# Performance work log

Hardware: AMD Instinct MI355X
Metric: run time of the kernel (lower is better)

Reference implementation:

```python
import jax, jax.numpy as jnp
import numpy as np

KNN = 16
BN_EPS = 1e-5


def _swiglu(z, w1, w2, w3):
    # SwiGLU applied over the last dim: w2(silu(w1 z) * (w3 z))
    return (jax.nn.silu(z @ w1.T) * (z @ w3.T)) @ w2.T


def setup_inputs() -> dict:
    key = jax.random.key(0)
    ks = jax.random.split(key, 12)
    B, T, D = 1, 2048, 768
    H, N, KD = 4, 25600, 128
    HID_A, HID_S = 44, 1024
    inp = {
        "x": jax.random.normal(ks[0], (B, T, D), jnp.float32),
        "wq": jax.random.normal(ks[1], (H * KD, D), jnp.float32) * (1.0 / np.sqrt(D)),
        "bq": jax.random.normal(ks[2], (H * KD,), jnp.float32) * 0.02,
        "bn_gamma": jnp.ones((H * KD,), jnp.float32),
        "bn_beta": jnp.zeros((H * KD,), jnp.float32),
        "bn_mean": jnp.zeros((H * KD,), jnp.float32),
        "bn_var": jnp.ones((H * KD,), jnp.float32),
        "keys": jax.random.uniform(ks[3], (H, N, KD), jnp.float32, -1.0 / np.sqrt(KD), 1.0 / np.sqrt(KD)),
        "w_down_tab": jax.random.normal(ks[4], (N, 1), jnp.float32) * 0.02,
        "w_up_tab": jax.random.normal(ks[5], (N, 1), jnp.float32) * 0.02,
        "a_w1": jax.random.normal(ks[6], (HID_A, KNN), jnp.float32) * (1.0 / np.sqrt(KNN)),
        "a_w2": jax.random.normal(ks[7], (KNN, HID_A), jnp.float32) * (1.0 / np.sqrt(HID_A)),
        "a_w3": jax.random.normal(ks[8], (HID_A, KNN), jnp.float32) * (1.0 / np.sqrt(KNN)),
        "s_w1": jax.random.normal(ks[9], (HID_S, D), jnp.float32) * (1.0 / np.sqrt(D)),
        "s_w2": jax.random.normal(ks[10], (D, HID_S), jnp.float32) * (1.0 / np.sqrt(HID_S)),
        "s_w3": jax.random.normal(ks[11], (HID_S, D), jnp.float32) * (1.0 / np.sqrt(D)),
    }
    return inp


def reference(x, wq, bq, bn_gamma, bn_beta, bn_mean, bn_var, keys,
              w_down_tab, w_up_tab, a_w1, a_w2, a_w3, s_w1, s_w2, s_w3):
    B, T, D = x.shape
    H, N, KD = keys.shape
    identity = x
    # query projection + BatchNorm1d (inference: running stats)
    q = x.reshape(-1, D) @ wq.T + bq                      # (bs, H*KD)
    q = (q - bn_mean) * jax.lax.rsqrt(bn_var + BN_EPS) * bn_gamma + bn_beta
    q = q.reshape(-1, H, KD)                              # (bs, H, KD)
    # product-key scoring against full key table, per head
    scores = jnp.einsum('bhk,hnk->bhn', q, keys)          # (bs, H, N)
    top_s, top_i = jax.lax.top_k(scores, KNN)             # (bs, H, KNN)
    gates = jax.nn.softmax(top_s, axis=-1)
    idx = top_i.reshape(B, T, H, KNN)
    gates = gates.reshape(B, T, H, KNN)
    # expert_dim == 1: embedding gather yields a scalar per selected expert
    w_down = w_down_tab[idx, 0]                           # (B, T, H, KNN)
    w_up = w_up_tab[idx, 0]                               # (B, T, H, KNN)
    # einsum('btd,bthkd->bthk') with d-broadcast (expert_dim=1 vs D):
    # equals sum_d x[b,t,d] * w_down[b,t,h,k,0]
    xd = jnp.sum(x, axis=-1)[:, :, None, None] * w_down   # (B, T, H, KNN)
    h = _swiglu(xd, a_w1, a_w2, a_w3)                     # (B, T, H, KNN)
    h = h * gates
    # einsum('bthk,bthkd->btd') with d=1 -> (B, T, 1), broadcasts vs (B,T,D)
    comb = jnp.sum(h * w_up, axis=(2, 3))[:, :, None]     # (B, T, 1)
    out = comb + _swiglu(identity, s_w1, s_w2, s_w3)      # (B, T, D)
    return out
```

## Files before the change

kernel.cpp:

```cpp
#include <hip/hip_runtime.h>
#include <hip/hip_bf16.h>
#include <cmath>

#define NEG_INF (-3.402823466e38f)
#define SPLITS 32
#define SPN    800
#define GRP    32
#define NGRP   25

typedef __attribute__((ext_vector_type(8))) short s16x8;
typedef __attribute__((ext_vector_type(4))) float f32x4;

__device__ __forceinline__ unsigned short f2bf(float f) {
    union { float f; unsigned u; } v; v.f = f;
    unsigned u = v.u;
    u += 0x7fffu + ((u >> 16) & 1u);
    return (unsigned short)(u >> 16);
}

__global__ __launch_bounds__(256) void cvt_small_kernel(
        const float* __restrict__ s0, const float* __restrict__ s1,
        const float* __restrict__ s2, const float* __restrict__ s3,
        const float* __restrict__ s4,
        unsigned short* __restrict__ dst, float* __restrict__ sumx) {
    int i = blockIdx.x * 256 + threadIdx.x;
    const float* src; int base;
    if      (i < 393216)  { src = s0;   base = 0; }
    else if (i < 491520)  { src = s1;   base = 393216; }
    else if (i < 688128)  { src = s2;   base = 491520; }
    else if (i < 884736)  { src = s3;   base = 688128; }
    else                  { src = s4;   base = 884736; }
    float4 f = ((const float4*)src)[i - base];
    ushort4 o;
    o.x = f2bf(f.x); o.y = f2bf(f.y); o.z = f2bf(f.z); o.w = f2bf(f.w);
    ((ushort4*)dst)[i] = o;
    if (i < 393216) {
        float s = f.x + f.y + f.z + f.w;
        #pragma unroll
        for (int off = 32; off > 0; off >>= 1) s += __shfl_down(s, off);
        if ((threadIdx.x & 63) == 0) atomicAdd(&sumx[i / 192], s);
    }
}

__device__ __forceinline__ void qproj_body(
        int sb, int tid, const unsigned short* __restrict__ A,
        const unsigned short* __restrict__ W, unsigned short* __restrict__ outB,
        const float* __restrict__ bq, const float* __restrict__ gamma,
        const float* __restrict__ beta, const float* __restrict__ mean,
        const float* __restrict__ var, char* smem) {
    short (*As)[72] = (short(*)[72])smem;
    short (*Ws)[72] = (short(*)[72])(smem + 9216);
    const int m0 = (sb & 31) * 64, n0 = (sb >> 5) * 64;
    const int wv = tid >> 6, lane = tid & 63;
    const int wr = wv >> 1, wc = wv & 1;
    const int lr = lane & 15, lq = lane >> 4;
    f32x4 acc[2][2];
    #pragma unroll
    for (int i = 0; i < 2; ++i)
        #pragma unroll
        for (int j = 0; j < 2; ++j) acc[i][j] = (f32x4){0.f, 0.f, 0.f, 0.f};
    for (int kb = 0; kb < 768; kb += 64) {
        #pragma unroll
        for (int it = 0; it < 2; ++it) {
            int chunk = tid + it * 256;
            int row = chunk >> 3, c8 = (chunk & 7) * 8;
            *(s16x8*)&As[row][c8] = *(const s16x8*)(A + (size_t)(m0 + row) * 768 + kb + c8);
            *(s16x8*)&Ws[row][c8] = *(const s16x8*)(W + (size_t)(n0 + row) * 768 + kb + c8);
        }
        __syncthreads();
        #pragma unroll
        for (int ks = 0; ks < 2; ++ks) {
            const int k0 = ks * 32 + lq * 8;
            #pragma unroll
            for (int rt = 0; rt < 2; ++rt) {
                s16x8 a = *(const s16x8*)&As[wr * 32 + rt * 16 + lr][k0];
                #pragma unroll
                for (int ct = 0; ct < 2; ++ct) {
                    s16x8 b = *(const s16x8*)&Ws[wc * 32 + ct * 16 + lr][k0];
                    acc[rt][ct] = __builtin_amdgcn_mfma_f32_16x16x32_bf16(a, b, acc[rt][ct], 0, 0, 0);
                }
            }
        }
        __syncthreads();
    }
    #pragma unroll
    for (int rt = 0; rt < 2; ++rt)
        #pragma unroll
        for (int ct = 0; ct < 2; ++ct)
            #pragma unroll
            for (int r = 0; r < 4; ++r) {
                int m = m0 + wr * 32 + rt * 16 + lq * 4 + r;
                int n = n0 + wc * 32 + ct * 16 + lr;
                float q = acc[rt][ct][r] + bq[n];
                q = (q - mean[n]) * rsqrtf(var[n] + 1e-5f) * gamma[n] + beta[n];
                outB[(size_t)m * 512 + n] = f2bf(q);
            }
}

__global__ __launch_bounds__(256) void megaQ_kernel(
        const unsigned short* __restrict__ xb, const unsigned short* __restrict__ wqb,
        unsigned short* __restrict__ qb,
        const float* __restrict__ bq, const float* __restrict__ gamma,
        const float* __restrict__ beta, const float* __restrict__ mean,
        const float* __restrict__ var,
        const float* __restrict__ keys, unsigned short* __restrict__ keys_b) {
    __shared__ alignas(16) char smem[18432];
    if (blockIdx.x < 256) {
        qproj_body(blockIdx.x, threadIdx.x, xb, wqb, qb, bq, gamma, beta,
                   mean, var, smem);
    } else {
        int i = (blockIdx.x - 256) * 256 + threadIdx.x;
        float4 f = ((const float4*)keys)[i];
        ushort4 o;
        o.x = f2bf(f.x); o.y = f2bf(f.y); o.z = f2bf(f.z); o.w = f2bf(f.w);
        ((ushort4*)keys_b)[i] = o;
    }
}

template <int EPI>
__global__ __launch_bounds__(256) void gemm_nt(
        const unsigned short* __restrict__ A, const unsigned short* __restrict__ W,
        int M, int N, int K,
        float* __restrict__ outF, unsigned short* __restrict__ outB,
        const float* __restrict__ p0) {
    __shared__ alignas(16) short As[64][72];
    __shared__ alignas(16) short Ws[64][72];
    const int tid = threadIdx.x;
    const int m0 = blockIdx.x * 64, n0 = blockIdx.y * 64;
    const int wv = tid >> 6, lane = tid & 63;
    const int wr = wv >> 1, wc = wv & 1;
    const int lr = lane & 15, lq = lane >> 4;
    f32x4 acc[2][2];
    #pragma unroll
    for (int i = 0; i < 2; ++i)
        #pragma unroll
        for (int j = 0; j < 2; ++j) acc[i][j] = (f32x4){0.f, 0.f, 0.f, 0.f};

    for (int kb = 0; kb < K; kb += 64) {
        #pragma unroll
        for (int it = 0; it < 2; ++it) {
            int chunk = tid + it * 256;
            int row = chunk >> 3, c8 = (chunk & 7) * 8;
            *(s16x8*)&As[row][c8] = *(const s16x8*)(A + (size_t)(m0 + row) * K + kb + c8);
            *(s16x8*)&Ws[row][c8] = *(const s16x8*)(W + (size_t)(n0 + row) * K + kb + c8);
        }
        __syncthreads();
        #pragma unroll
        for (int ks = 0; ks < 2; ++ks) {
            const int k0 = ks * 32 + lq * 8;
            #pragma unroll
            for (int rt = 0; rt < 2; ++rt) {
                s16x8 a = *(const s16x8*)&As[wr * 32 + rt * 16 + lr][k0];
                #pragma unroll
                for (int ct = 0; ct < 2; ++ct) {
                    s16x8 b = *(const s16x8*)&Ws[wc * 32 + ct * 16 + lr][k0];
                    acc[rt][ct] = __builtin_amdgcn_mfma_f32_16x16x32_bf16(a, b, acc[rt][ct], 0, 0, 0);
                }
            }
        }
        __syncthreads();
    }
    #pragma unroll
    for (int rt = 0; rt < 2; ++rt)
        #pragma unroll
        for (int ct = 0; ct < 2; ++ct)
            #pragma unroll
            for (int r = 0; r < 4; ++r) {
                int m = m0 + wr * 32 + rt * 16 + lq * 4 + r;
                int n = n0 + wc * 32 + ct * 16 + lr;
                outF[(size_t)m * N + n] = acc[rt][ct][r] + p0[m];
            }
}

__device__ __forceinline__ void swiglu_body(
        int sb, int tid, const unsigned short* __restrict__ A,
        const unsigned short* __restrict__ W1, const unsigned short* __restrict__ W3,
        unsigned short* __restrict__ outB, char* smem) {
    short (*As)[72]  = (short(*)[72])smem;
    short (*W1s)[72] = (short(*)[72])(smem + 9216);
    short (*W3s)[72] = (short(*)[72])(smem + 18432);
    const int m0 = (sb & 31) * 64, n0 = (sb >> 5) * 64;
    const int wv = tid >> 6, lane = tid & 63;
    const int wr = wv >> 1, wc = wv & 1;
    const int lr = lane & 15, lq = lane >> 4;
    f32x4 acc1[2][2], acc3[2][2];
    #pragma unroll
    for (int i = 0; i < 2; ++i)
        #pragma unroll
        for (int j = 0; j < 2; ++j) {
            acc1[i][j] = (f32x4){0.f, 0.f, 0.f, 0.f};
            acc3[i][j] = (f32x4){0.f, 0.f, 0.f, 0.f};
        }
    for (int kb = 0; kb < 768; kb += 64) {
        #pragma unroll
        for (int it = 0; it < 2; ++it) {
            int chunk = tid + it * 256;
            int row = chunk >> 3, c8 = (chunk & 7) * 8;
            *(s16x8*)&As[row][c8]  = *(const s16x8*)(A  + (size_t)(m0 + row) * 768 + kb + c8);
            *(s16x8*)&W1s[row][c8] = *(const s16x8*)(W1 + (size_t)(n0 + row) * 768 + kb + c8);
            *(s16x8*)&W3s[row][c8] = *(const s16x8*)(W3 + (size_t)(n0 + row) * 768 + kb + c8);
        }
        __syncthreads();
        #pragma unroll
        for (int ks = 0; ks < 2; ++ks) {
            const int k0 = ks * 32 + lq * 8;
            #pragma unroll
            for (int rt = 0; rt < 2; ++rt) {
                s16x8 a = *(const s16x8*)&As[wr * 32 + rt * 16 + lr][k0];
                #pragma unroll
                for (int ct = 0; ct < 2; ++ct) {
                    s16x8 b1 = *(const s16x8*)&W1s[wc * 32 + ct * 16 + lr][k0];
                    s16x8 b3 = *(const s16x8*)&W3s[wc * 32 + ct * 16 + lr][k0];
                    acc1[rt][ct] = __builtin_amdgcn_mfma_f32_16x16x32_bf16(a, b1, acc1[rt][ct], 0, 0, 0);
                    acc3[rt][ct] = __builtin_amdgcn_mfma_f32_16x16x32_bf16(a, b3, acc3[rt][ct], 0, 0, 0);
                }
            }
        }
        __syncthreads();
    }
    #pragma unroll
    for (int rt = 0; rt < 2; ++rt)
        #pragma unroll
        for (int ct = 0; ct < 2; ++ct)
            #pragma unroll
            for (int r = 0; r < 4; ++r) {
                int m = m0 + wr * 32 + rt * 16 + lq * 4 + r;
                int n = n0 + wc * 32 + ct * 16 + lr;
                float u1 = acc1[rt][ct][r], u3 = acc3[rt][ct][r];
                float hv = u1 / (1.f + expf(-u1)) * u3;
                outB[(size_t)m * 1024 + n] = f2bf(hv);
            }
}

__device__ __forceinline__ void down_body(
        int sb, int tid, const unsigned short* __restrict__ A,
        const unsigned short* __restrict__ W, float* __restrict__ outF,
        char* smem) {
    short (*As)[72] = (short(*)[72])smem;
    short (*Ws)[72] = (short(*)[72])(smem + 9216);
    const int m0 = (sb & 31) * 64, n0 = (sb >> 5) * 64;
    const int wv = tid >> 6, lane = tid & 63;
    const int wr = wv >> 1, wc = wv & 1;
    const int lr = lane & 15, lq = lane >> 4;
    f32x4 acc[2][2];
    #pragma unroll
    for (int i = 0; i < 2; ++i)
        #pragma unroll
        for (int j = 0; j < 2; ++j) acc[i][j] = (f32x4){0.f, 0.f, 0.f, 0.f};
    for (int kb = 0; kb < 1024; kb += 64) {
        #pragma unroll
        for (int it = 0; it < 2; ++it) {
            int chunk = tid + it * 256;
            int row = chunk >> 3, c8 = (chunk & 7) * 8;
            *(s16x8*)&As[row][c8] = *(const s16x8*)(A + (size_t)(m0 + row) * 1024 + kb + c8);
            *(s16x8*)&Ws[row][c8] = *(const s16x8*)(W + (size_t)(n0 + row) * 1024 + kb + c8);
        }
        __syncthreads();
        #pragma unroll
        for (int ks = 0; ks < 2; ++ks) {
            const int k0 = ks * 32 + lq * 8;
            #pragma unroll
            for (int rt = 0; rt < 2; ++rt) {
                s16x8 a = *(const s16x8*)&As[wr * 32 + rt * 16 + lr][k0];
                #pragma unroll
                for (int ct = 0; ct < 2; ++ct) {
                    s16x8 b = *(const s16x8*)&Ws[wc * 32 + ct * 16 + lr][k0];
                    acc[rt][ct] = __builtin_amdgcn_mfma_f32_16x16x32_bf16(a, b, acc[rt][ct], 0, 0, 0);
                }
            }
        }
        __syncthreads();
    }
    #pragma unroll
    for (int rt = 0; rt < 2; ++rt)
        #pragma unroll
        for (int ct = 0; ct < 2; ++ct)
            #pragma unroll
            for (int r = 0; r < 4; ++r) {
                int m = m0 + wr * 32 + rt * 16 + lq * 4 + r;
                int n = n0 + wc * 32 + ct * 16 + lr;
                outF[(size_t)m * 768 + n] = acc[rt][ct][r];
            }
}

template <int PASS>
__device__ __forceinline__ void score_body(
        int b, int tid,
        const unsigned short* __restrict__ Q, const unsigned short* __restrict__ Kt,
        float* __restrict__ maxbuf, const float* __restrict__ theta,
        int* __restrict__ cnt, float2* __restrict__ buf, char* smem) {
    short (*Ks)[GRP][136] = (short(*)[GRP][136])smem;
    const int tile = b >> 7;
    const int hsp = b & 127;
    const int h = hsp >> 5, sp = hsp & 31;
    const int w = tid >> 6, lane = tid & 63;
    const int lr = lane & 15, lq = lane >> 4;
    const int t0 = tile * 256 + w * 64;
    const int nb0 = sp * SPN;

    s16x8 qf[4][4];
    #pragma unroll
    for (int tt = 0; tt < 4; ++tt) {
        const unsigned short* qp = Q + (size_t)(t0 + tt * 16 + lr) * 512 + h * 128 + lq * 8;
        #pragma unroll
        for (int ks = 0; ks < 4; ++ks) qf[tt][ks] = *(const s16x8*)(qp + ks * 32);
    }

    float runmax[4] = {NEG_INF, NEG_INF, NEG_INF, NEG_INF};
    float th[4];
    if (PASS == 2) {
        #pragma unroll
        for (int tt = 0; tt < 4; ++tt) th[tt] = theta[(t0 + tt * 16 + lr) * 4 + h];
    }

    const int srow = tid >> 4;
    const int scol = (tid & 15) * 8;
    const unsigned short* kgp =
        Kt + ((size_t)h * 25600 + nb0 + srow) * 128 + scol;

    {
        *(s16x8*)&Ks[0][srow][scol]      = *(const s16x8*)kgp;
        *(s16x8*)&Ks[0][srow + 16][scol] = *(const s16x8*)(kgp + 2048);
    }

    for (int g = 0; g < NGRP; ++g) {
        s16x8 ka0, ka1;
        if (g + 1 < NGRP) {
            const unsigned short* kp = kgp + (size_t)(g + 1) * 4096;
            ka0 = *(const s16x8*)kp;
            ka1 = *(const s16x8*)(kp + 2048);
        }
        __syncthreads();
        const int cb = g & 1;
        #pragma unroll
        for (int st = 0; st < 2; ++st) {
            f32x4 acc[4];
            #pragma unroll
            for (int tt = 0; tt < 4; ++tt) acc[tt] = (f32x4){0.f, 0.f, 0.f, 0.f};
            #pragma unroll
            for (int ks = 0; ks < 4; ++ks) {
                s16x8 ka = *(const s16x8*)&Ks[cb][st * 16 + lr][ks * 32 + lq * 8];
                #pragma unroll
                for (int tt = 0; tt < 4; ++tt)
                    acc[tt] = __builtin_amdgcn_mfma_f32_16x16x32_bf16(ka, qf[tt][ks], acc[tt], 0, 0, 0);
            }
            if (PASS == 1) {
                #pragma unroll
                for (int tt = 0; tt < 4; ++tt) {
                    float m0 = fmaxf(fmaxf(acc[tt][0], acc[tt][1]),
                                     fmaxf(acc[tt][2], acc[tt][3]));
                    runmax[tt] = fmaxf(runmax[tt], m0);
                }
            } else {
                const int nb = nb0 + g * GRP + st * 16;
                #pragma unroll
                for (int tt = 0; tt < 4; ++tt) {
                    float m0 = fmaxf(fmaxf(acc[tt][0], acc[tt][1]),
                                     fmaxf(acc[tt][2], acc[tt][3]));
                    if (m0 >= th[tt]) {
                        int g4 = (t0 + tt * 16 + lr) * 4 + h;
                        #pragma unroll
                        for (int r = 0; r < 4; ++r) {
                            if (acc[tt][r] >= th[tt]) {
                                int n = nb + lq * 4 + r;
                                int pos = atomicAdd(&cnt[g4], 1);
                                if (pos < 64) {
                                    float2 e; e.x = acc[tt][r]; e.y = __int_as_float(n);
                                    buf[(size_t)g4 * 64 + pos] = e;
                                }
                            }
                        }
                    }
                }
            }
        }
        if (g + 1 < NGRP) {
            const int nbuf = cb ^ 1;
            *(s16x8*)&Ks[nbuf][srow][scol]      = ka0;
            *(s16x8*)&Ks[nbuf][srow + 16][scol] = ka1;
        }
    }

    if (PASS == 1) {
        #pragma unroll
        for (int tt = 0; tt < 4; ++tt)
            maxbuf[(size_t)((t0 + tt * 16 + lr) * 4 + h) * 128 + sp * 4 + lq] = runmax[tt];
    }
}

template <int PASS>
__global__ __launch_bounds__(256, 4) void score_pass_kernel(
        const unsigned short* __restrict__ Q, const unsigned short* __restrict__ Kt,
        float* __restrict__ maxbuf, const float* __restrict__ theta,
        int* __restrict__ cnt, float2* __restrict__ buf) {
    __shared__ alignas(16) char smem[17408];
    score_body<PASS>(blockIdx.x, threadIdx.x, Q, Kt, maxbuf, theta, cnt, buf, smem);
}

__global__ __launch_bounds__(256, 4) void megaA_kernel(
        const unsigned short* __restrict__ xb, const unsigned short* __restrict__ w1,
        const unsigned short* __restrict__ w3, unsigned short* __restrict__ hb,
        const unsigned short* __restrict__ Q, const unsigned short* __restrict__ Kt,
        float* __restrict__ maxbuf) {
    __shared__ alignas(16) char smem[27648];
    if (blockIdx.x < 512)
        swiglu_body(blockIdx.x, threadIdx.x, xb, w1, w3, hb, smem);
    else
        score_body<1>(blockIdx.x - 512, threadIdx.x, Q, Kt, maxbuf,
                      nullptr, nullptr, nullptr, smem);
}

__global__ __launch_bounds__(256, 4) void megaB_kernel(
        const unsigned short* __restrict__ hb, const unsigned short* __restrict__ w2,
        float* __restrict__ outF,
        const unsigned short* __restrict__ Q, const unsigned short* __restrict__ Kt,
        const float* __restrict__ theta, int* __restrict__ cnt,
        float2* __restrict__ buf) {
    __shared__ alignas(16) char smem[18432];
    if (blockIdx.x < 384)
        down_body(blockIdx.x, threadIdx.x, hb, w2, outF, smem);
    else
        score_body<2>(blockIdx.x - 384, threadIdx.x, Q, Kt, nullptr,
                      theta, cnt, buf, smem);
}

__global__ __launch_bounds__(64) void theta_kernel(
        const float* __restrict__ maxbuf, float* __restrict__ theta) {
    int g = blockIdx.x * 64 + threadIdx.x;
    if (g >= 8192) return;
    const float* mb = maxbuf + (size_t)g * 128;
    float s[16];
    #pragma unroll
    for (int i = 0; i < 16; ++i) s[i] = NEG_INF;
    for (int j = 0; j < 128; ++j) {
        float v = mb[j];
        if (v > s[15]) {
            #pragma unroll
            for (int i = 15; i > 0; --i)
                s[i] = (v > s[i - 1]) ? s[i - 1] : ((v > s[i]) ? v : s[i]);
            s[0] = (v > s[0]) ? v : s[0];
        }
    }
    theta[g] = s[15];
}

template <int FUSE_OUT>
__global__ __launch_bounds__(256) void finalize_kernel(
        const int* __restrict__ cnt, const float2* __restrict__ buf,
        const float* __restrict__ sumx,
        const float* __restrict__ wdown, const float* __restrict__ wup,
        const float* __restrict__ aw1, const float* __restrict__ aw2,
        const float* __restrict__ aw3, float* __restrict__ combsum,
        float* __restrict__ out) {
    __shared__ float zsh[4][16];
    __shared__ float wsh[4][16];
    __shared__ float csh[4];
    const int wv = threadIdx.x >> 6, lane = threadIdx.x & 63;
    const int t = blockIdx.x;
    const int g = t * 4 + wv;
    int c = cnt[g]; c = (c > 64) ? 64 : c;

    float v = NEG_INF; int n = 0x7fffffff;
    if (lane < c) {
        float2 e = buf[(size_t)g * 64 + lane];
        v = e.x; n = __float_as_int(e.y);
    }
    int r = 0;
    for (int i = 0; i < c; ++i) {
        float vi = __shfl(v, i);
        int   ni = __shfl(n, i);
        r += ((vi > v) || (vi == v && ni < n)) ? 1 : 0;
    }
    float m = v;
    #pragma unroll
    for (int off = 32; off > 0; off >>= 1) m = fmaxf(m, __shfl_xor(m, off));
    const bool sel = (lane < c) && (r < 16);
    float e = sel ? expf(v - m) : 0.f;
    float den = e;
    #pragma unroll
    for (int off = 32; off > 0; off >>= 1) den += __shfl_xor(den, off);
    if (sel) {
        zsh[wv][r] = sumx[t] * wdown[n];
        wsh[wv][r] = (e / den) * wup[n];
    }
    __syncthreads();
    float contrib = 0.f;
    if (lane < 44) {
        float u1 = 0.f, u3 = 0.f, cj = 0.f;
        #pragma unroll
        for (int k = 0; k < 16; ++k) {
            float zk = zsh[wv][k];
            u1 += zk * aw1[lane * 16 + k];
            u3 += zk * aw3[lane * 16 + k];
            cj += wsh[wv][k] * aw2[k * 44 + lane];
        }
        float gj = u1 / (1.f + expf(-u1)) * u3;
        contrib = gj * cj;
    }
    #pragma unroll
    for (int off = 32; off > 0; off >>= 1) contrib += __shfl_xor(contrib, off);
    if (FUSE_OUT) {
        if (lane == 0) csh[wv] = contrib;
        __syncthreads();
        float comb = csh[0] + csh[1] + csh[2] + csh[3];
        float* orow = out + (size_t)t * 768;
        #pragma unroll
        for (int i = 0; i < 3; ++i) orow[threadIdx.x + i * 256] += comb;
    } else {
        if (lane == 0) atomicAdd(&combsum[t], contrib);
    }
}

__global__ __launch_bounds__(256) void gemm_swiglu_kernel(
        const unsigned short* __restrict__ A, const unsigned short* __restrict__ W1,
        const unsigned short* __restrict__ W3, unsigned short* __restrict__ outB) {
    __shared__ alignas(16) char smem[27648];
    swiglu_body(blockIdx.x, threadIdx.x, A, W1, W3, outB, smem);
}

extern "C" void kernel_launch(void* const* d_in, const int* in_sizes, int n_in,
                              void* d_out, int out_size, void* d_ws, size_t ws_size,
                              hipStream_t stream) {
    const float* x     = (const float*)d_in[0];
    const float* wq    = (const float*)d_in[1];
    const float* bq    = (const float*)d_in[2];
    const float* gamma = (const float*)d_in[3];
    const float* beta  = (const float*)d_in[4];
    const float* mean  = (const float*)d_in[5];
    const float* var   = (const float*)d_in[6];
    const float* keys  = (const float*)d_in[7];
    const float* wdown = (const float*)d_in[8];
    const float* wup   = (const float*)d_in[9];
    const float* aw1   = (const float*)d_in[10];
    const float* aw2   = (const float*)d_in[11];
    const float* aw3   = (const float*)d_in[12];
    const float* sw1   = (const float*)d_in[13];
    const float* sw2   = (const float*)d_in[14];
    const float* sw3   = (const float*)d_in[15];
    float* out = (float*)d_out;

    char* ws = (char*)d_ws;
    unsigned short* x_b    = (unsigned short*)(ws + 0);
    unsigned short* wq_b   = (unsigned short*)(ws + 3145728);
    unsigned short* sw1_b  = (unsigned short*)(ws + 3932160);
    unsigned short* sw3_b  = (unsigned short*)(ws + 5505024);
    unsigned short* sw2_b  = (unsigned short*)(ws + 7077888);
    unsigned short* keys_b = (unsigned short*)(ws + 8650752);
    unsigned short* q_b    = (unsigned short*)(ws + 34865152);
    float* sumx    = (float*)(ws + 36962304);
    float* theta   = (float*)(ws + 36970496);
    float* combsum = (float*)(ws + 37003264);
    int*   cnt     = (int*)  (ws + 37011456);
    char* R1 = ws + 37044224;
    float* maxbuf = (float*)R1;
    float2* buf   = (float2*)R1;
    unsigned short* h_b_fused = (unsigned short*)(ws + 41238528);
    const bool fused = ws_size >= 45432832ull;

    hipMemsetAsync(ws + 36962304, 0, 81920, stream);
    cvt_small_kernel<<<4224, 256, 0, stream>>>(x, wq, sw1, sw3, sw2, x_b, sumx);
    megaQ_kernel<<<13056, 256, 0, stream>>>(x_b, wq_b, q_b, bq, gamma, beta,
                                            mean, var, keys, keys_b);
    if (fused) {
        megaA_kernel<<<1536, 256, 0, stream>>>(x_b, sw1_b, sw3_b, h_b_fused,
                                               q_b, keys_b, maxbuf);
        theta_kernel<<<128, 64, 0, stream>>>(maxbuf, theta);
        megaB_kernel<<<1408, 256, 0, stream>>>(h_b_fused, sw2_b, out,
                                               q_b, keys_b, theta, cnt, buf);
        finalize_kernel<1><<<2048, 256, 0, stream>>>(cnt, buf, sumx, wdown, wup,
                                                     aw1, aw2, aw3, combsum, out);
    } else {
        unsigned short* h_b = (unsigned short*)R1;
        score_pass_kernel<1><<<1024, 256, 0, stream>>>(q_b, keys_b, maxbuf, nullptr, nullptr, nullptr);
        theta_kernel<<<128, 64, 0, stream>>>(maxbuf, theta);
        score_pass_kernel<2><<<1024, 256, 0, stream>>>(q_b, keys_b, nullptr, theta, cnt, buf);
        finalize_kernel<0><<<2048, 256, 0, stream>>>(cnt, buf, sumx, wdown, wup,
                                                     aw1, aw2, aw3, combsum, nullptr);
        gemm_swiglu_kernel<<<512, 256, 0, stream>>>(x_b, sw1_b, sw3_b, h_b);
        gemm_nt<2><<<dim3(32, 12), 256, 0, stream>>>(h_b, sw2_b, 2048, 768, 1024,
                                                     out, nullptr, combsum);
    }
}
```

Before: 298.9 us.

## Skip score sub-tiles below threshold using pass-1 submaxima; fold conversions into Q kernel

Pass 1 of the top-k scoring now records a per-warp, per-16-key sub-tile maximum. Pass 2 skips the MFMA scoring for any sub-tile whose maximum is below the smallest threshold among the warp's tokens. This cuts most pass-2 compute, at the cost of an extra submax buffer and a larger workspace requirement. The separate conversion kernel is folded into the Q-projection kernel, which now reads fp32 x and wq and converts them on the fly, saving a launch. The maxbuf layout is also transposed so theta_kernel's loads coalesce.

Result: slower. 339.1 us (+13.4%).

```diff
diff --git a/kernel.cpp b/kernel.cpp
--- a/kernel.cpp
+++ b/kernel.cpp
@@ -18,33 +18,18 @@
     return (unsigned short)(u >> 16);
 }
 
-__global__ __launch_bounds__(256) void cvt_small_kernel(
-        const float* __restrict__ s0, const float* __restrict__ s1,
-        const float* __restrict__ s2, const float* __restrict__ s3,
-        const float* __restrict__ s4,
-        unsigned short* __restrict__ dst, float* __restrict__ sumx) {
-    int i = blockIdx.x * 256 + threadIdx.x;
-    const float* src; int base;
-    if      (i < 393216)  { src = s0;   base = 0; }
-    else if (i < 491520)  { src = s1;   base = 393216; }
-    else if (i < 688128)  { src = s2;   base = 491520; }
-    else if (i < 884736)  { src = s3;   base = 688128; }
-    else                  { src = s4;   base = 884736; }
-    float4 f = ((const float4*)src)[i - base];
-    ushort4 o;
-    o.x = f2bf(f.x); o.y = f2bf(f.y); o.z = f2bf(f.z); o.w = f2bf(f.w);
-    ((ushort4*)dst)[i] = o;
-    if (i < 393216) {
-        float s = f.x + f.y + f.z + f.w;
-        #pragma unroll
-        for (int off = 32; off > 0; off >>= 1) s += __shfl_down(s, off);
-        if ((threadIdx.x & 63) == 0) atomicAdd(&sumx[i / 192], s);
-    }
+__device__ __forceinline__ s16x8 pack8(float4 a, float4 b) {
+    s16x8 v;
+    v[0] = (short)f2bf(a.x); v[1] = (short)f2bf(a.y);
+    v[2] = (short)f2bf(a.z); v[3] = (short)f2bf(a.w);
+    v[4] = (short)f2bf(b.x); v[5] = (short)f2bf(b.y);
+    v[6] = (short)f2bf(b.z); v[7] = (short)f2bf(b.w);
+    return v;
 }
 
 __device__ __forceinline__ void qproj_body(
-        int sb, int tid, const unsigned short* __restrict__ A,
-        const unsigned short* __restrict__ W, unsigned short* __restrict__ outB,
+        int sb, int tid, const float* __restrict__ A, const float* __restrict__ W,
+        unsigned short* __restrict__ outB,
         const float* __restrict__ bq, const float* __restrict__ gamma,
         const float* __restrict__ beta, const float* __restrict__ mean,
         const float* __restrict__ var, char* smem) {
@@ -64,8 +49,10 @@
         for (int it = 0; it < 2; ++it) {
             int chunk = tid + it * 256;
             int row = chunk >> 3, c8 = (chunk & 7) * 8;
-            *(s16x8*)&As[row][c8] = *(const s16x8*)(A + (size_t)(m0 + row) * 768 + kb + c8);
-            *(s16x8*)&Ws[row][c8] = *(const s16x8*)(W + (size_t)(n0 + row) * 768 + kb + c8);
+            const float* ap = A + (size_t)(m0 + row) * 768 + kb + c8;
+            const float* wp = W + (size_t)(n0 + row) * 768 + kb + c8;
+            *(s16x8*)&As[row][c8] = pack8(*(const float4*)ap, *(const float4*)(ap + 4));
+            *(s16x8*)&Ws[row][c8] = pack8(*(const float4*)wp, *(const float4*)(wp + 4));
         }
         __syncthreads();
         #pragma unroll
@@ -97,31 +84,52 @@
             }
 }
 
-__global__ __launch_bounds__(256) void megaQ_kernel(
-        const unsigned short* __restrict__ xb, const unsigned short* __restrict__ wqb,
+__global__ __launch_bounds__(256) void megaQ2_kernel(
+        const float* __restrict__ x, const float* __restrict__ wq,
         unsigned short* __restrict__ qb,
         const float* __restrict__ bq, const float* __restrict__ gamma,
         const float* __restrict__ beta, const float* __restrict__ mean,
         const float* __restrict__ var,
-        const float* __restrict__ keys, unsigned short* __restrict__ keys_b) {
+        const float* __restrict__ keys, unsigned short* __restrict__ keys_b,
+        const float* __restrict__ sw1, const float* __restrict__ sw3,
+        const float* __restrict__ sw2,
+        unsigned short* __restrict__ x_b, unsigned short* __restrict__ sw1_b,
+        unsigned short* __restrict__ sw3_b, unsigned short* __restrict__ sw2_b,
+        float* __restrict__ sumx) {
     __shared__ alignas(16) char smem[18432];
     if (blockIdx.x < 256) {
-        qproj_body(blockIdx.x, threadIdx.x, xb, wqb, qb, bq, gamma, beta,
+        qproj_body(blockIdx.x, threadIdx.x, x, wq, qb, bq, gamma, beta,
                    mean, var, smem);
-    } else {
+    } else if (blockIdx.x < 13056) {
         int i = (blockIdx.x - 256) * 256 + threadIdx.x;
         float4 f = ((const float4*)keys)[i];
         ushort4 o;
         o.x = f2bf(f.x); o.y = f2bf(f.y); o.z = f2bf(f.z); o.w = f2bf(f.w);
         ((ushort4*)keys_b)[i] = o;
-    }
-}
-
-template <int EPI>
-__global__ __launch_bounds__(256) void gemm_nt(
+    } else {
+        int j = (blockIdx.x - 13056) * 256 + threadIdx.x;
+        const float* src; unsigned short* dst; int base;
+        if      (j < 393216) { src = x;   dst = x_b;   base = 0; }
+        else if (j < 589824) { src = sw1; dst = sw1_b; base = 393216; }
+        else if (j < 786432) { src = sw3; dst = sw3_b; base = 589824; }
+        else                 { src = sw2; dst = sw2_b; base = 786432; }
+        int k = j - base;
+        float4 f = ((const float4*)src)[k];
+        ushort4 o;
+        o.x = f2bf(f.x); o.y = f2bf(f.y); o.z = f2bf(f.z); o.w = f2bf(f.w);
+        ((ushort4*)dst)[k] = o;
+        if (j < 393216) {
+            float s = f.x + f.y + f.z + f.w;
+            #pragma unroll
+            for (int off = 32; off > 0; off >>= 1) s += __shfl_down(s, off);
+            if ((threadIdx.x & 63) == 0) atomicAdd(&sumx[j / 192], s);
+        }
+    }
+}
+
+__global__ __launch_bounds__(256) void gemm_nt2(
         const unsigned short* __restrict__ A, const unsigned short* __restrict__ W,
-        int M, int N, int K,
-        float* __restrict__ outF, unsigned short* __restrict__ outB,
+        int M, int N, int K, float* __restrict__ outF,
         const float* __restrict__ p0) {
     __shared__ alignas(16) short As[64][72];
     __shared__ alignas(16) short Ws[64][72];
@@ -135,7 +143,6 @@
     for (int i = 0; i < 2; ++i)
         #pragma unroll
         for (int j = 0; j < 2; ++j) acc[i][j] = (f32x4){0.f, 0.f, 0.f, 0.f};
-
     for (int kb = 0; kb < K; kb += 64) {
         #pragma unroll
         for (int it = 0; it < 2; ++it) {
@@ -283,12 +290,13 @@
             }
 }
 
-template <int PASS>
+template <int PASS, int SKIP>
 __device__ __forceinline__ void score_body(
         int b, int tid,
         const unsigned short* __restrict__ Q, const unsigned short* __restrict__ Kt,
         float* __restrict__ maxbuf, const float* __restrict__ theta,
-        int* __restrict__ cnt, float2* __restrict__ buf, char* smem) {
+        int* __restrict__ cnt, float2* __restrict__ buf,
+        float* __restrict__ submax, char* smem) {
     short (*Ks)[GRP][136] = (short(*)[GRP][136])smem;
     const int tile = b >> 7;
     const int hsp = b & 127;
@@ -308,10 +316,20 @@
 
     float runmax[4] = {NEG_INF, NEG_INF, NEG_INF, NEG_INF};
     float th[4];
+    float thmin = NEG_INF;
     if (PASS == 2) {
         #pragma unroll
         for (int tt = 0; tt < 4; ++tt) th[tt] = theta[(t0 + tt * 16 + lr) * 4 + h];
-    }
+        if (SKIP) {
+            thmin = fminf(fminf(th[0], th[1]), fminf(th[2], th[3]));
+            #pragma unroll
+            for (int off = 32; off > 0; off >>= 1)
+                thmin = fminf(thmin, __shfl_xor(thmin, off));
+        }
+    }
+    const size_t sbase = ((size_t)b * 4 + w) * 50;
+    float smc0 = 0.f, smc1 = 0.f;
+    if (PASS == 2 && SKIP) { smc0 = submax[sbase]; smc1 = submax[sbase + 1]; }
 
     const int srow = tid >> 4;
     const int scol = (tid & 15) * 8;
@@ -325,15 +343,24 @@
 
     for (int g = 0; g < NGRP; ++g) {
         s16x8 ka0, ka1;
+        float smn0 = 0.f, smn1 = 0.f;
         if (g + 1 < NGRP) {
             const unsigned short* kp = kgp + (size_t)(g + 1) * 4096;
             ka0 = *(const s16x8*)kp;
             ka1 = *(const s16x8*)(kp + 2048);
+            if (PASS == 2 && SKIP) {
+                smn0 = submax[sbase + (g + 1) * 2];
+                smn1 = submax[sbase + (g + 1) * 2 + 1];
+            }
         }
         __syncthreads();
         const int cb = g & 1;
         #pragma unroll
         for (int st = 0; st < 2; ++st) {
+            if (PASS == 2 && SKIP) {
+                float sm = (st == 0) ? smc0 : smc1;
+                if (sm < thmin) continue;
+            }
             f32x4 acc[4];
             #pragma unroll
             for (int tt = 0; tt < 4; ++tt) acc[tt] = (f32x4){0.f, 0.f, 0.f, 0.f};
@@ -345,11 +372,19 @@
                     acc[tt] = __builtin_amdgcn_mfma_f32_16x16x32_bf16(ka, qf[tt][ks], acc[tt], 0, 0, 0);
             }
             if (PASS == 1) {
+                float m0s[4];
                 #pragma unroll
                 for (int tt = 0; tt < 4; ++tt) {
-                    float m0 = fmaxf(fmaxf(acc[tt][0], acc[tt][1]),
-                                     fmaxf(acc[tt][2], acc[tt][3]));
-                    runmax[tt] = fmaxf(runmax[tt], m0);
+                    m0s[tt] = fmaxf(fmaxf(acc[tt][0], acc[tt][1]),
+                                    fmaxf(acc[tt][2], acc[tt][3]));
+                    runmax[tt] = fmaxf(runmax[tt], m0s[tt]);
+                }
+                if (SKIP) {
+                    float sm = fmaxf(fmaxf(m0s[0], m0s[1]), fmaxf(m0s[2], m0s[3]));
+                    #pragma unroll
+                    for (int off = 32; off > 0; off >>= 1)
+                        sm = fmaxf(sm, __shfl_xor(sm, off));
+                    if (lane == 0) submax[sbase + g * 2 + st] = sm;
                 }
             } else {
                 const int nb = nb0 + g * GRP + st * 16;
@@ -378,13 +413,14 @@
             const int nbuf = cb ^ 1;
             *(s16x8*)&Ks[nbuf][srow][scol]      = ka0;
             *(s16x8*)&Ks[nbuf][srow + 16][scol] = ka1;
+            if (PASS == 2 && SKIP) { smc0 = smn0; smc1 = smn1; }
         }
     }
 
     if (PASS == 1) {
         #pragma unroll
         for (int tt = 0; tt < 4; ++tt)
-            maxbuf[(size_t)((t0 + tt * 16 + lr) * 4 + h) * 128 + sp * 4 + lq] = runmax[tt];
+            maxbuf[(size_t)(sp * 4 + lq) * 8192 + (t0 + tt * 16 + lr) * 4 + h] = runmax[tt];
     }
 }
 
@@ -394,20 +430,21 @@
         float* __restrict__ maxbuf, const float* __restrict__ theta,
         int* __restrict__ cnt, float2* __restrict__ buf) {
     __shared__ alignas(16) char smem[17408];
-    score_body<PASS>(blockIdx.x, threadIdx.x, Q, Kt, maxbuf, theta, cnt, buf, smem);
+    score_body<PASS, 0>(blockIdx.x, threadIdx.x, Q, Kt, maxbuf, theta, cnt, buf,
+                        nullptr, smem);
 }
 
 __global__ __launch_bounds__(256, 4) void megaA_kernel(
         const unsigned short* __restrict__ xb, const unsigned short* __restrict__ w1,
         const unsigned short* __restrict__ w3, unsigned short* __restrict__ hb,
         const unsigned short* __restrict__ Q, const unsigned short* __restrict__ Kt,
-        float* __restrict__ maxbuf) {
+        float* __restrict__ maxbuf, float* __restrict__ submax) {
     __shared__ alignas(16) char smem[27648];
     if (blockIdx.x < 512)
         swiglu_body(blockIdx.x, threadIdx.x, xb, w1, w3, hb, smem);
     else
-        score_body<1>(blockIdx.x - 512, threadIdx.x, Q, Kt, maxbuf,
-                      nullptr, nullptr, nullptr, smem);
+        score_body<1, 1>(blockIdx.x - 512, threadIdx.x, Q, Kt, maxbuf,
+                         nullptr, nullptr, nullptr, submax, smem);
 }
 
 __global__ __launch_bounds__(256, 4) void megaB_kernel(
@@ -415,25 +452,25 @@
         float* __restrict__ outF,
         const unsigned short* __restrict__ Q, const unsigned short* __restrict__ Kt,
         const float* __restrict__ theta, int* __restrict__ cnt,
-        float2* __restrict__ buf) {
+        float2* __restrict__ buf, float* __restrict__ submax) {
     __shared__ alignas(16) char smem[18432];
     if (blockIdx.x < 384)
         down_body(blockIdx.x, threadIdx.x, hb, w2, outF, smem);
     else
-        score_body<2>(blockIdx.x - 384, threadIdx.x, Q, Kt, nullptr,
-                      theta, cnt, buf, smem);
+        score_body<2, 1>(blockIdx.x - 384, threadIdx.x, Q, Kt, nullptr,
+                         theta, cnt, buf, submax, smem);
 }
 
 __global__ __launch_bounds__(64) void theta_kernel(
         const float* __restrict__ maxbuf, float* __restrict__ theta) {
     int g = blockIdx.x * 64 + threadIdx.x;
     if (g >= 8192) return;
-    const float* mb = maxbuf + (size_t)g * 128;
+    const float* mb = maxbuf + g;
     float s[16];
     #pragma unroll
     for (int i = 0; i < 16; ++i) s[i] = NEG_INF;
     for (int j = 0; j < 128; ++j) {
-        float v = mb[j];
+        float v = mb[(size_t)j * 8192];
         if (v > s[15]) {
             #pragma unroll
             for (int i = 15; i > 0; --i)
@@ -541,7 +578,6 @@
 
     char* ws = (char*)d_ws;
     unsigned short* x_b    = (unsigned short*)(ws + 0);
-    unsigned short* wq_b   = (unsigned short*)(ws + 3145728);
     unsigned short* sw1_b  = (unsigned short*)(ws + 3932160);
     unsigned short* sw3_b  = (unsigned short*)(ws + 5505024);
     unsigned short* sw2_b  = (unsigned short*)(ws + 7077888);
@@ -555,18 +591,20 @@
     float* maxbuf = (float*)R1;
     float2* buf   = (float2*)R1;
     unsigned short* h_b_fused = (unsigned short*)(ws + 41238528);
-    const bool fused = ws_size >= 45432832ull;
+    float* submax = (float*)(ws + 45432832);
+    const bool fused = ws_size >= 46252032ull;
 
     hipMemsetAsync(ws + 36962304, 0, 81920, stream);
-    cvt_small_kernel<<<4224, 256, 0, stream>>>(x, wq, sw1, sw3, sw2, x_b, sumx);
-    megaQ_kernel<<<13056, 256, 0, stream>>>(x_b, wq_b, q_b, bq, gamma, beta,
-                                            mean, var, keys, keys_b);
+    megaQ2_kernel<<<16896, 256, 0, stream>>>(x, wq, q_b, bq, gamma, beta,
+                                             mean, var, keys, keys_b,
+                                             sw1, sw3, sw2,
+                                             x_b, sw1_b, sw3_b, sw2_b, sumx);
     if (fused) {
         megaA_kernel<<<1536, 256, 0, stream>>>(x_b, sw1_b, sw3_b, h_b_fused,
-                                               q_b, keys_b, maxbuf);
+                                               q_b, keys_b, maxbuf, submax);
         theta_kernel<<<128, 64, 0, stream>>>(maxbuf, theta);
         megaB_kernel<<<1408, 256, 0, stream>>>(h_b_fused, sw2_b, out,
-                                               q_b, keys_b, theta, cnt, buf);
+                                               q_b, keys_b, theta, cnt, buf, submax);
         finalize_kernel<1><<<2048, 256, 0, stream>>>(cnt, buf, sumx, wdown, wup,
                                                      aw1, aw2, aw3, combsum, out);
     } else {
@@ -577,7 +615,7 @@
         finalize_kernel<0><<<2048, 256, 0, stream>>>(cnt, buf, sumx, wdown, wup,
                                                      aw1, aw2, aw3, combsum, nullptr);
         gemm_swiglu_kernel<<<512, 256, 0, stream>>>(x_b, sw1_b, sw3_b, h_b);
-        gemm_nt<2><<<dim3(32, 12), 256, 0, stream>>>(h_b, sw2_b, 2048, 768, 1024,
-                                                     out, nullptr, combsum);
-    }
-}
+        gemm_nt2<<<dim3(32, 12), 256, 0, stream>>>(h_b, sw2_b, 2048, 768, 1024,
+                                                   out, combsum);
+    }
+}
```
